# Kernel optimization log

Measured on AMD Instinct MI355X. Metric: run time of the kernel, lower is better.

The kernel has to match this reference:

```python
import jax, jax.numpy as jnp
import numpy as np

BOUND = 1.0
DENSITY_SCALE = 1.0
MIN_NEAR = 0.2
EPS = 1e-15


def setup_inputs() -> dict:
    key = jax.random.key(0)
    ks = jax.random.split(key, 10)
    N, H = 32768, 32
    rays_o = (jax.random.uniform(ks[0], (N, 3), jnp.float32) - 0.5)  # inside AABB
    rays_d = jax.random.normal(ks[1], (N, 3), jnp.float32)
    W1 = jax.random.normal(ks[2], (3, H), jnp.float32) * 0.5
    b1 = jnp.zeros((H,), jnp.float32)
    Wsig = jax.random.normal(ks[3], (H, 1), jnp.float32) * 0.5
    Wsig_d = jax.random.normal(ks[4], (H, 1), jnp.float32) * 0.5
    Wc1 = jax.random.normal(ks[5], (6, H), jnp.float32) * 0.5
    bc1 = jnp.zeros((H,), jnp.float32)
    Wc2 = jax.random.normal(ks[6], (H, 3), jnp.float32) * 0.5
    Wc2_d = jax.random.normal(ks[7], (H, 3), jnp.float32) * 0.5
    return {"rays_o": rays_o, "rays_d": rays_d, "W1": W1, "b1": b1,
            "Wsig": Wsig, "Wsig_d": Wsig_d, "Wc1": Wc1, "bc1": bc1,
            "Wc2": Wc2, "Wc2_d": Wc2_d, "num_steps": 128}


def _composite(deltas, sigma, z01, rgbs):
    # alphas / transmittance / weights, as in run()
    alphas = 1.0 - jnp.exp(-deltas * DENSITY_SCALE * sigma)           # [N,T]
    shifted = jnp.concatenate([jnp.ones_like(alphas[..., :1]),
                               1.0 - alphas + EPS], axis=-1)
    weights = alphas * jnp.cumprod(shifted, axis=-1)[..., :-1]        # [N,T]
    ws = weights.sum(axis=-1)                                          # [N]
    depth = jnp.sum(weights * z01, axis=-1)                            # [N]
    image = jnp.sum(weights[..., None] * rgbs, axis=-2)                # [N,3]
    image = image + (1.0 - ws)[..., None] * 1.0  # bg_color = 1
    return image, depth, ws


def reference(rays_o, rays_d, W1, b1, Wsig, Wsig_d, Wc1, bc1, Wc2, Wc2_d, num_steps):
    N = rays_o.shape[0]
    T = num_steps
    d = rays_d / jnp.linalg.norm(rays_d, axis=-1, keepdims=True)
    # near_far_from_aabb (slab test), aabb = [-1,1]^3
    inv = 1.0 / d
    t1 = (-BOUND - rays_o) * inv
    t2 = (BOUND - rays_o) * inv
    near = jnp.max(jnp.minimum(t1, t2), axis=-1, keepdims=True)        # [N,1]
    far = jnp.min(jnp.maximum(t1, t2), axis=-1, keepdims=True)
    near = jnp.maximum(near, MIN_NEAR)
    far = jnp.maximum(far, near + 1e-6)
    z = jnp.linspace(0.0, 1.0, T, dtype=rays_o.dtype)[None, :]
    z_vals = near + (far - near) * z                                    # [N,T]
    sample_dist = (far - near) / T                                      # [N,1]
    xyzs = rays_o[:, None, :] + d[:, None, :] * z_vals[..., None]       # [N,T,3]
    xyzs = jnp.clip(xyzs, -BOUND, BOUND)
    # surrogate density MLP (shared trunk, main + dummy heads)
    h = jax.nn.relu(jnp.einsum('ntc,ch->nth', xyzs, W1) + b1)           # [N,T,H]
    sigma = jax.nn.softplus(jnp.einsum('nth,ho->nt', h, Wsig))          # [N,T]
    sigma_dummy = jax.nn.softplus(jnp.einsum('nth,ho->nt', h, Wsig_d))
    # deltas
    deltas = z_vals[..., 1:] - z_vals[..., :-1]
    deltas = jnp.concatenate([deltas, sample_dist * jnp.ones_like(deltas[..., :1])], axis=-1)
    # surrogate color MLP on (xyz, dir)
    dirs = jnp.broadcast_to(d[:, None, :], xyzs.shape)
    feat = jnp.concatenate([xyzs, dirs], axis=-1)                       # [N,T,6]
    hc = jax.nn.relu(jnp.einsum('ntc,ch->nth', feat, Wc1) + bc1)
    rgbs = jax.nn.sigmoid(jnp.einsum('nth,hc->ntc', hc, Wc2))           # [N,T,3]
    rgbs_dummy = jax.nn.sigmoid(jnp.einsum('nth,hc->ntc', hc, Wc2_d))
    z01 = jnp.clip((z_vals - near) / (far - near), 0.0, 1.0)
    image, depth, ws = _composite(deltas, sigma, z01, rgbs)
    image_d, depth_d, _ = _composite(deltas, sigma_dummy, z01, rgbs_dummy)
    # pack: image(3) | depth(1) | weights_sum(1) | image_dummy(3) | depth_dummy(1)
    return jnp.concatenate([image, depth[:, None], ws[:, None],
                            image_d, depth_d[:, None]], axis=-1)        # [N,9]
```

## Files before the change

### kernel.cpp

```cpp
#include <hip/hip_runtime.h>
#include <hip/hip_bf16.h>


typedef float  f32x4  __attribute__((ext_vector_type(4)));
typedef short  bf16x8 __attribute__((ext_vector_type(8)));
typedef unsigned int u32;

__device__ __forceinline__ float fast_rcp(float x){ return __builtin_amdgcn_rcpf(x); }
__device__ __forceinline__ float softplus_f(float x){
    float e = __expf(-fabsf(x));
    return fmaxf(x,0.f) + __logf(1.f+e);
}
__device__ __forceinline__ float sigmoid_f(float x){ return fast_rcp(1.f+__expf(-x)); }

__device__ __forceinline__ u32 pkrn(float lo, float hi){
    const u32 a = __float_as_uint(lo) + 0x8000u;
    const u32 b = __float_as_uint(hi) + 0x8000u;
    return __builtin_amdgcn_perm(b, a, 0x07060302u);
}
__device__ __forceinline__ u32 bfr_hi(float f){
    u32 u = __float_as_uint(f);
    return (u + 0x7FFFu + ((u>>16)&1u)) & 0xFFFF0000u;
}
__device__ __forceinline__ u32 pkbf(float lo, float hi){
    return (bfr_hi(lo)>>16) | bfr_hi(hi);
}

__global__ __launch_bounds__(256)
void nerf_prep_kernel(const float* __restrict__ W1, const float* __restrict__ b1,
                      const float* __restrict__ Wsig, const float* __restrict__ Wsig_d,
                      const float* __restrict__ Wc1, const float* __restrict__ bc1,
                      const float* __restrict__ Wc2, const float* __restrict__ Wc2_d,
                      u32* __restrict__ ws)
{
    const int q0 = threadIdx.x;
#pragma unroll
    for (int k = 0; k < 6; ++k) {
        const int q = q0 + k*256;
        u32 val = 0u;
        if (q < 1024) {
            const int ut = q>>8, rem = q&255, lane = rem>>2, dw = rem&3;
            const int g = lane>>4, m = lane&15;
            if (g == 0) {
                float w[8];
                if (ut < 2) { const int u = ut*16 + m;
                    w[0]=W1[u];  w[1]=W1[32+u];  w[2]=W1[64+u];  w[3]=b1[u];
                    w[4]=0.f;    w[5]=0.f;       w[6]=0.f;       w[7]=0.f;
                } else {        const int u = (ut-2)*16 + m;
                    w[0]=Wc1[u]; w[1]=Wc1[32+u]; w[2]=Wc1[64+u]; w[3]=bc1[u];
                    w[4]=Wc1[96+u]; w[5]=Wc1[128+u]; w[6]=Wc1[160+u]; w[7]=0.f;
                }
                val = pkbf(w[2*dw], w[2*dw+1]);
            }
        } else {
            const int q2 = q-1024, ch = q2>>8, rem = q2&255, lane = rem>>2, dw = rem&3;
            const int g = lane>>4, o = lane&15;
            float w[2];
#pragma unroll
            for (int e = 0; e < 2; ++e) {
                const int kk = 2*dw + e;
                const int h = kk>>2, rr = kk&3;
                const int u_local = h*16 + g*4 + rr;
                float v = 0.f;
                if (ch == 0) {
                    if (o == 0) v = Wsig[u_local];
                    else if (o == 1) v = Wsig_d[u_local];
                } else {
                    if (o >= 2 && o <= 4) v = Wc2[u_local*3 + (o-2)];
                    else if (o >= 5 && o <= 7) v = Wc2_d[u_local*3 + (o-5)];
                }
                w[e] = v;
            }
            val = pkbf(w[0], w[1]);
        }
        ws[q] = val;
    }
}

#define PSTR 8
#define SSTR 20
#define WSTR 1792
#define CSTR 100

__global__ __launch_bounds__(512, 4)
void nerf_render_kernel(const float* __restrict__ rays_o,
                        const float* __restrict__ rays_d,
                        const u32*  __restrict__ wsm,
                        const int*  __restrict__ num_steps,
                        float* __restrict__ out,
                        int N)
{
    __shared__ u32 smem[8 * WSTR];

    const int tid  = threadIdx.x;
    const int seg  = tid>>6, lane = tid&63;
    const int ray  = blockIdx.x*64 + lane;
    const int rayc = (ray < N) ? ray : (N-1);
    const int T = num_steps[0];
    const int g = lane>>4, c = lane&15;

    u32*   posW   = smem + seg*WSTR;
    float* stashW = (float*)(smem + seg*WSTR + 64*PSTR);
    float* comb   = (float*)smem;

    const uint4* wsv = (const uint4*)wsm;
    uint4 a1u0 = wsv[0*64 + lane];
    uint4 a1u1 = wsv[1*64 + lane];
    uint4 a1u2 = wsv[2*64 + lane];
    uint4 a1u3 = wsv[3*64 + lane];
    uint4 a2u0 = wsv[256 + 0*64 + lane];
    uint4 a2u1 = wsv[256 + 1*64 + lane];
    asm volatile("" : "+v"(a1u0.x), "+v"(a1u0.y), "+v"(a1u0.z), "+v"(a1u0.w),
                      "+v"(a1u1.x), "+v"(a1u1.y), "+v"(a1u1.z), "+v"(a1u1.w),
                      "+v"(a1u2.x), "+v"(a1u2.y), "+v"(a1u2.z), "+v"(a1u2.w));
    asm volatile("" : "+v"(a1u3.x), "+v"(a1u3.y), "+v"(a1u3.z), "+v"(a1u3.w),
                      "+v"(a2u0.x), "+v"(a2u0.y), "+v"(a2u0.z), "+v"(a2u0.w),
                      "+v"(a2u1.x), "+v"(a2u1.y), "+v"(a2u1.z), "+v"(a2u1.w));

    const float ox = rays_o[rayc*3+0], oy = rays_o[rayc*3+1], oz = rays_o[rayc*3+2];
    const float rdx = rays_d[rayc*3+0], rdy = rays_d[rayc*3+1], rdz = rays_d[rayc*3+2];
    const float rn = rsqrtf(rdx*rdx + rdy*rdy + rdz*rdz);
    const float dx = rdx*rn, dy = rdy*rn, dz = rdz*rn;

    const float ix = 1.0f/dx, iy = 1.0f/dy, iz = 1.0f/dz;
    const float t1x = (-1.f-ox)*ix, t2x = (1.f-ox)*ix;
    const float t1y = (-1.f-oy)*iy, t2y = (1.f-oy)*iy;
    const float t1z = (-1.f-oz)*iz, t2z = (1.f-oz)*iz;
    float nearv = fmaxf(fmaxf(fminf(t1x,t2x), fminf(t1y,t2y)), fminf(t1z,t2z));
    float farv  = fminf(fminf(fmaxf(t1x,t2x), fmaxf(t1y,t2y)), fmaxf(t1z,t2z));
    nearv = fmaxf(nearv, 0.2f);
    farv  = fmaxf(farv, nearv + 1e-6f);

    const float span    = farv - nearv;
    const float stepz   = (T > 1) ? span/(float)(T-1) : 0.f;
    const float inv_tm1 = (T > 1) ? 1.f/(float)(T-1) : 0.f;
    const float last_dt = span/(float)T;

    const u32 dirw0 = pkbf(dx, dy);
    const u32 dirw1 = pkbf(dz, 0.f);

    const int Sper = (T + 7) >> 3;
    const int segStart = seg * Sper;
    const int segEnd = (segStart + Sper < T) ? (segStart + Sper) : T;
    const int nch = (segEnd > segStart) ? ((segEnd - segStart + 1) >> 1) : 0;

    const int posOff = 4*c;
    const int stOff  = (c>>1)*SSTR + (c&1)*8 + g*4;

    float iA0=0.f,iA1=0.f,iA2=0.f,dAc=0.f,wsA=0.f,TAx=1.f;
    float iD0=0.f,iD1=0.f,iD2=0.f,dDc=0.f,wsD=0.f,TDx=1.f;

    for (int cs = 0; cs < nch; ++cs) {
        const int t0 = segStart + cs*2;

#pragma unroll
        for (int i = 0; i < 2; ++i) {
            const float zv = fmaf(stepz, (float)(t0 + i), nearv);
            const float X = fminf(fmaxf(fmaf(dx, zv, ox), -1.f), 1.f);
            const float Y = fminf(fmaxf(fmaf(dy, zv, oy), -1.f), 1.f);
            const float Z = fminf(fmaxf(fmaf(dz, zv, oz), -1.f), 1.f);
            uint4 v;
            v.x = pkrn(X, Y);
            v.y = pkrn(Z, 1.0f);
            v.z = dirw0;
            v.w = dirw1;
            *(uint4*)&posW[lane*PSTR + i*4] = v;
        }

#define TILEB(TAU)                                                                \
        {                                                                         \
            const uint4 b1u = *(const uint4*)&posW[(TAU)*(8*PSTR) + posOff];      \
            const bf16x8 b1f = __builtin_bit_cast(bf16x8, b1u);                   \
            f32x4 acc10 = __builtin_amdgcn_mfma_f32_16x16x32_bf16(                \
                __builtin_bit_cast(bf16x8, a1u0), b1f,(f32x4){0.f,0.f,0.f,0.f},0,0,0);\
            f32x4 acc11 = __builtin_amdgcn_mfma_f32_16x16x32_bf16(                \
                __builtin_bit_cast(bf16x8, a1u1), b1f,(f32x4){0.f,0.f,0.f,0.f},0,0,0);\
            f32x4 acc12 = __builtin_amdgcn_mfma_f32_16x16x32_bf16(                \
                __builtin_bit_cast(bf16x8, a1u2), b1f,(f32x4){0.f,0.f,0.f,0.f},0,0,0);\
            f32x4 acc13 = __builtin_amdgcn_mfma_f32_16x16x32_bf16(                \
                __builtin_bit_cast(bf16x8, a1u3), b1f,(f32x4){0.f,0.f,0.f,0.f},0,0,0);\
            const u32 p00 = pkrn(fmaxf(acc10.x,0.f), fmaxf(acc10.y,0.f));         \
            const u32 p10 = pkrn(fmaxf(acc10.z,0.f), fmaxf(acc10.w,0.f));         \
            const u32 p01 = pkrn(fmaxf(acc11.x,0.f), fmaxf(acc11.y,0.f));         \
            const u32 p11 = pkrn(fmaxf(acc11.z,0.f), fmaxf(acc11.w,0.f));         \
            const u32 p02 = pkrn(fmaxf(acc12.x,0.f), fmaxf(acc12.y,0.f));         \
            const u32 p12 = pkrn(fmaxf(acc12.z,0.f), fmaxf(acc12.w,0.f));         \
            const u32 p03 = pkrn(fmaxf(acc13.x,0.f), fmaxf(acc13.y,0.f));         \
            const u32 p13 = pkrn(fmaxf(acc13.z,0.f), fmaxf(acc13.w,0.f));         \
            uint4 b2a; b2a.x = p00; b2a.y = p10; b2a.z = p01; b2a.w = p11;        \
            uint4 b2b; b2b.x = p02; b2b.y = p12; b2b.z = p03; b2b.w = p13;        \
            f32x4 acc2 = __builtin_amdgcn_mfma_f32_16x16x32_bf16(                 \
                __builtin_bit_cast(bf16x8, a2u0), __builtin_bit_cast(bf16x8, b2a),\
                (f32x4){0.f,0.f,0.f,0.f}, 0, 0, 0);                               \
            acc2 = __builtin_amdgcn_mfma_f32_16x16x32_bf16(                       \
                __builtin_bit_cast(bf16x8, a2u1), __builtin_bit_cast(bf16x8, b2b),\
                acc2, 0, 0, 0);                                                   \
            if (g < 2) {                                                          \
                *(f32x4*)&stashW[(TAU)*(8*SSTR) + stOff] = acc2;                  \
            }                                                                     \
        }
        TILEB(0) TILEB(1) TILEB(2) TILEB(3)
        TILEB(4) TILEB(5) TILEB(6) TILEB(7)
#undef TILEB

#pragma unroll
        for (int t = 0; t < 2; ++t) {
            const int tg = t0 + t;
            if (tg < segEnd) {
                const f32x4 oA = *(const f32x4*)&stashW[lane*SSTR + t*8];
                const f32x4 oB = *(const f32x4*)&stashW[lane*SSTR + t*8 + 4];
                const float dneg = (tg < T-1) ? -stepz : -last_dt;
                const float z01  = (float)tg * inv_tm1;

                const float sigA = softplus_f(oA.x);
                const float qA = __expf(dneg*sigA);
                const float wA = TAx - TAx*qA; TAx *= qA;
                iA0 = fmaf(wA, sigmoid_f(oA.z), iA0);
                iA1 = fmaf(wA, sigmoid_f(oA.w), iA1);
                iA2 = fmaf(wA, sigmoid_f(oB.x), iA2);
                dAc = fmaf(wA, z01, dAc); wsA += wA;

                const float sigD = softplus_f(oA.y);
                const float qD = __expf(dneg*sigD);
                const float wD = TDx - TDx*qD; TDx *= qD;
                iD0 = fmaf(wD, sigmoid_f(oB.y), iD0);
                iD1 = fmaf(wD, sigmoid_f(oB.z), iD1);
                iD2 = fmaf(wD, sigmoid_f(oB.w), iD2);
                dDc = fmaf(wD, z01, dDc); wsD += wD;
            }
        }
    }

    __syncthreads();
    *(f32x4*)&comb[lane*CSTR + seg*12 + 0] = (f32x4){iA0, iA1, iA2, dAc};
    *(f32x4*)&comb[lane*CSTR + seg*12 + 4] = (f32x4){wsA, TAx, iD0, iD1};
    *(f32x4*)&comb[lane*CSTR + seg*12 + 8] = (f32x4){iD2, dDc, wsD, TDx};
    __syncthreads();

    if (seg == 0) {
        float tA = TAx, tD = TDx;
#pragma unroll
        for (int s = 1; s < 8; ++s) {
            const f32x4 v0 = *(const f32x4*)&comb[lane*CSTR + s*12 + 0];
            const f32x4 v1 = *(const f32x4*)&comb[lane*CSTR + s*12 + 4];
            const f32x4 v2 = *(const f32x4*)&comb[lane*CSTR + s*12 + 8];
            iA0 = fmaf(tA, v0.x, iA0);
            iA1 = fmaf(tA, v0.y, iA1);
            iA2 = fmaf(tA, v0.z, iA2);
            dAc = fmaf(tA, v0.w, dAc);
            wsA = fmaf(tA, v1.x, wsA);
            tA *= v1.y;
            iD0 = fmaf(tD, v1.z, iD0);
            iD1 = fmaf(tD, v1.w, iD1);
            iD2 = fmaf(tD, v2.x, iD2);
            dDc = fmaf(tD, v2.y, dDc);
            wsD = fmaf(tD, v2.z, wsD);
            tD *= v2.w;
        }
        if (ray < N) {
            const float bgA = 1.f - wsA;
            const float bgD = 1.f - wsD;
            float* o = out + (size_t)ray * 9;
            o[0] = iA0 + bgA;
            o[1] = iA1 + bgA;
            o[2] = iA2 + bgA;
            o[3] = dAc;
            o[4] = wsA;
            o[5] = iD0 + bgD;
            o[6] = iD1 + bgD;
            o[7] = iD2 + bgD;
            o[8] = dDc;
        }
    }
}

extern "C" void kernel_launch(void* const* d_in, const int* in_sizes, int n_in,
                              void* d_out, int out_size, void* d_ws, size_t ws_size,
                              hipStream_t stream) {
    const float* rays_o = (const float*)d_in[0];
    const float* rays_d = (const float*)d_in[1];
    const float* W1     = (const float*)d_in[2];
    const float* b1     = (const float*)d_in[3];
    const float* Wsig   = (const float*)d_in[4];
    const float* Wsig_d = (const float*)d_in[5];
    const float* Wc1    = (const float*)d_in[6];
    const float* bc1    = (const float*)d_in[7];
    const float* Wc2    = (const float*)d_in[8];
    const float* Wc2_d  = (const float*)d_in[9];
    const int* num_steps = (const int*)d_in[10];

    const int N = in_sizes[0] / 3;
    float* out = (float*)d_out;
    u32*   ws  = (u32*)d_ws;

    hipLaunchKernelGGL(nerf_prep_kernel, dim3(1), dim3(256), 0, stream,
                       W1, b1, Wsig, Wsig_d, Wc1, bc1, Wc2, Wc2_d, ws);

    const int blocks = (N + 63) / 64;
    hipLaunchKernelGGL(nerf_render_kernel, dim3(blocks), dim3(512), 0, stream,
                       rays_o, rays_d, ws, num_steps, out, N);
}
```

Measured before the change: 57.24 us.

## Split ray samples across two blocks and combine partials in separate kernel

The render kernel now uses 256-thread blocks, each handling half of the sample range of 64 rays. Partial composite state (accumulations plus transmittance) goes to workspace, and a new combine kernel merges the two halves. The aim is smaller blocks, higher occupancy and more blocks for scheduling. The cost is an extra kernel launch and a round trip of the partials through global memory. The ReLU/pack code is also rewritten using vector max, which is cosmetic.

```diff
diff --git a/kernel.cpp b/kernel.cpp
--- a/kernel.cpp
+++ b/kernel.cpp
@@ -80,21 +80,23 @@
 #define PSTR 8
 #define SSTR 20
 #define WSTR 1792
-#define CSTR 100
-
-__global__ __launch_bounds__(512, 4)
+#define CSTR 52
+#define PART_OFF 2048
+
+__global__ __launch_bounds__(256, 5)
 void nerf_render_kernel(const float* __restrict__ rays_o,
                         const float* __restrict__ rays_d,
                         const u32*  __restrict__ wsm,
                         const int*  __restrict__ num_steps,
-                        float* __restrict__ out,
+                        float* __restrict__ partials,
                         int N)
 {
-    __shared__ u32 smem[8 * WSTR];
+    __shared__ u32 smem[4 * WSTR];
 
     const int tid  = threadIdx.x;
     const int seg  = tid>>6, lane = tid&63;
-    const int ray  = blockIdx.x*64 + lane;
+    const int half = blockIdx.x & 1;
+    const int ray  = (blockIdx.x >> 1)*64 + lane;
     const int rayc = (ray < N) ? ray : (N-1);
     const int T = num_steps[0];
     const int g = lane>>4, c = lane&15;
@@ -139,9 +141,12 @@
     const u32 dirw0 = pkbf(dx, dy);
     const u32 dirw1 = pkbf(dz, 0.f);
 
-    const int Sper = (T + 7) >> 3;
-    const int segStart = seg * Sper;
-    const int segEnd = (segStart + Sper < T) ? (segStart + Sper) : T;
+    const int halfT = (T + 1) >> 1;
+    const int Sper  = (halfT + 3) >> 2;
+    const int hEnd  = ((half + 1)*halfT < T) ? (half + 1)*halfT : T;
+    const int segStart = half*halfT + seg*Sper;
+    int segEnd = segStart + Sper;
+    segEnd = (segEnd < hEnd) ? segEnd : hEnd;
     const int nch = (segEnd > segStart) ? ((segEnd - segStart + 1) >> 1) : 0;
 
     const int posOff = 4*c;
@@ -149,6 +154,7 @@
 
     float iA0=0.f,iA1=0.f,iA2=0.f,dAc=0.f,wsA=0.f,TAx=1.f;
     float iD0=0.f,iD1=0.f,iD2=0.f,dDc=0.f,wsD=0.f,TDx=1.f;
+    const f32x4 z4 = {0.f,0.f,0.f,0.f};
 
     for (int cs = 0; cs < nch; ++cs) {
         const int t0 = segStart + cs*2;
@@ -172,26 +178,25 @@
             const uint4 b1u = *(const uint4*)&posW[(TAU)*(8*PSTR) + posOff];      \
             const bf16x8 b1f = __builtin_bit_cast(bf16x8, b1u);                   \
             f32x4 acc10 = __builtin_amdgcn_mfma_f32_16x16x32_bf16(                \
-                __builtin_bit_cast(bf16x8, a1u0), b1f,(f32x4){0.f,0.f,0.f,0.f},0,0,0);\
+                __builtin_bit_cast(bf16x8, a1u0), b1f, z4, 0,0,0);                \
             f32x4 acc11 = __builtin_amdgcn_mfma_f32_16x16x32_bf16(                \
-                __builtin_bit_cast(bf16x8, a1u1), b1f,(f32x4){0.f,0.f,0.f,0.f},0,0,0);\
+                __builtin_bit_cast(bf16x8, a1u1), b1f, z4, 0,0,0);                \
             f32x4 acc12 = __builtin_amdgcn_mfma_f32_16x16x32_bf16(                \
-                __builtin_bit_cast(bf16x8, a1u2), b1f,(f32x4){0.f,0.f,0.f,0.f},0,0,0);\
+                __builtin_bit_cast(bf16x8, a1u2), b1f, z4, 0,0,0);                \
             f32x4 acc13 = __builtin_amdgcn_mfma_f32_16x16x32_bf16(                \
-                __builtin_bit_cast(bf16x8, a1u3), b1f,(f32x4){0.f,0.f,0.f,0.f},0,0,0);\
-            const u32 p00 = pkrn(fmaxf(acc10.x,0.f), fmaxf(acc10.y,0.f));         \
-            const u32 p10 = pkrn(fmaxf(acc10.z,0.f), fmaxf(acc10.w,0.f));         \
-            const u32 p01 = pkrn(fmaxf(acc11.x,0.f), fmaxf(acc11.y,0.f));         \
-            const u32 p11 = pkrn(fmaxf(acc11.z,0.f), fmaxf(acc11.w,0.f));         \
-            const u32 p02 = pkrn(fmaxf(acc12.x,0.f), fmaxf(acc12.y,0.f));         \
-            const u32 p12 = pkrn(fmaxf(acc12.z,0.f), fmaxf(acc12.w,0.f));         \
-            const u32 p03 = pkrn(fmaxf(acc13.x,0.f), fmaxf(acc13.y,0.f));         \
-            const u32 p13 = pkrn(fmaxf(acc13.z,0.f), fmaxf(acc13.w,0.f));         \
-            uint4 b2a; b2a.x = p00; b2a.y = p10; b2a.z = p01; b2a.w = p11;        \
-            uint4 b2b; b2b.x = p02; b2b.y = p12; b2b.z = p03; b2b.w = p13;        \
+                __builtin_bit_cast(bf16x8, a1u3), b1f, z4, 0,0,0);                \
+            const f32x4 r0 = __builtin_elementwise_max(acc10, z4);                \
+            const f32x4 r1 = __builtin_elementwise_max(acc11, z4);                \
+            const f32x4 r2 = __builtin_elementwise_max(acc12, z4);                \
+            const f32x4 r3 = __builtin_elementwise_max(acc13, z4);                \
+            uint4 b2a, b2b;                                                       \
+            b2a.x = pkrn(r0.x, r0.y);  b2a.y = pkrn(r0.z, r0.w);                  \
+            b2a.z = pkrn(r1.x, r1.y);  b2a.w = pkrn(r1.z, r1.w);                  \
+            b2b.x = pkrn(r2.x, r2.y);  b2b.y = pkrn(r2.z, r2.w);                  \
+            b2b.z = pkrn(r3.x, r3.y);  b2b.w = pkrn(r3.z, r3.w);                  \
             f32x4 acc2 = __builtin_amdgcn_mfma_f32_16x16x32_bf16(                 \
                 __builtin_bit_cast(bf16x8, a2u0), __builtin_bit_cast(bf16x8, b2a),\
-                (f32x4){0.f,0.f,0.f,0.f}, 0, 0, 0);                               \
+                z4, 0, 0, 0);                                                     \
             acc2 = __builtin_amdgcn_mfma_f32_16x16x32_bf16(                       \
                 __builtin_bit_cast(bf16x8, a2u1), __builtin_bit_cast(bf16x8, b2b),\
                 acc2, 0, 0, 0);                                                   \
@@ -237,10 +242,10 @@
     *(f32x4*)&comb[lane*CSTR + seg*12 + 8] = (f32x4){iD2, dDc, wsD, TDx};
     __syncthreads();
 
-    if (seg == 0) {
+    if (seg == 0 && ray < N) {
         float tA = TAx, tD = TDx;
 #pragma unroll
-        for (int s = 1; s < 8; ++s) {
+        for (int s = 1; s < 4; ++s) {
             const f32x4 v0 = *(const f32x4*)&comb[lane*CSTR + s*12 + 0];
             const f32x4 v1 = *(const f32x4*)&comb[lane*CSTR + s*12 + 4];
             const f32x4 v2 = *(const f32x4*)&comb[lane*CSTR + s*12 + 8];
@@ -257,21 +262,52 @@
             wsD = fmaf(tD, v2.z, wsD);
             tD *= v2.w;
         }
-        if (ray < N) {
-            const float bgA = 1.f - wsA;
-            const float bgD = 1.f - wsD;
-            float* o = out + (size_t)ray * 9;
-            o[0] = iA0 + bgA;
-            o[1] = iA1 + bgA;
-            o[2] = iA2 + bgA;
-            o[3] = dAc;
-            o[4] = wsA;
-            o[5] = iD0 + bgD;
-            o[6] = iD1 + bgD;
-            o[7] = iD2 + bgD;
-            o[8] = dDc;
-        }
+        float* pw = partials + (size_t)(half*N + ray)*12;
+        *(f32x4*)&pw[0] = (f32x4){iA0, iA1, iA2, dAc};
+        *(f32x4*)&pw[4] = (f32x4){wsA, tA, iD0, iD1};
+        *(f32x4*)&pw[8] = (f32x4){iD2, dDc, wsD, tD};
     }
+}
+
+__global__ __launch_bounds__(256)
+void nerf_combine_kernel(const float* __restrict__ partials,
+                         float* __restrict__ out, int N)
+{
+    const int ray = blockIdx.x*256 + threadIdx.x;
+    if (ray >= N) return;
+    const float* p0 = partials + (size_t)ray*12;
+    const float* p1 = partials + (size_t)(N + ray)*12;
+    const f32x4 a0 = *(const f32x4*)&p0[0];
+    const f32x4 a1 = *(const f32x4*)&p0[4];
+    const f32x4 a2 = *(const f32x4*)&p0[8];
+    const f32x4 b0 = *(const f32x4*)&p1[0];
+    const f32x4 b1 = *(const f32x4*)&p1[4];
+    const f32x4 b2 = *(const f32x4*)&p1[8];
+
+    const float TA0 = a1.y, TD0 = a2.w;
+    const float iA0 = a0.x + TA0*b0.x;
+    const float iA1 = a0.y + TA0*b0.y;
+    const float iA2 = a0.z + TA0*b0.z;
+    const float dAc = a0.w + TA0*b0.w;
+    const float wsA = a1.x + TA0*b1.x;
+    const float iD0 = a1.z + TD0*b1.z;
+    const float iD1 = a1.w + TD0*b1.w;
+    const float iD2 = a2.x + TD0*b2.x;
+    const float dDc = a2.y + TD0*b2.y;
+    const float wsD = a2.z + TD0*b2.z;
+
+    const float bgA = 1.f - wsA;
+    const float bgD = 1.f - wsD;
+    float* o = out + (size_t)ray * 9;
+    o[0] = iA0 + bgA;
+    o[1] = iA1 + bgA;
+    o[2] = iA2 + bgA;
+    o[3] = dAc;
+    o[4] = wsA;
+    o[5] = iD0 + bgD;
+    o[6] = iD1 + bgD;
+    o[7] = iD2 + bgD;
+    o[8] = dDc;
 }
 
 extern "C" void kernel_launch(void* const* d_in, const int* in_sizes, int n_in,
@@ -292,11 +328,16 @@
     const int N = in_sizes[0] / 3;
     float* out = (float*)d_out;
     u32*   ws  = (u32*)d_ws;
+    float* partials = (float*)((u32*)d_ws + PART_OFF);
 
     hipLaunchKernelGGL(nerf_prep_kernel, dim3(1), dim3(256), 0, stream,
                        W1, b1, Wsig, Wsig_d, Wc1, bc1, Wc2, Wc2_d, ws);
 
-    const int blocks = (N + 63) / 64;
-    hipLaunchKernelGGL(nerf_render_kernel, dim3(blocks), dim3(512), 0, stream,
-                       rays_o, rays_d, ws, num_steps, out, N);
-}
+    const int rblocks = ((N + 63) / 64) * 2;
+    hipLaunchKernelGGL(nerf_render_kernel, dim3(rblocks), dim3(256), 0, stream,
+                       rays_o, rays_d, ws, num_steps, partials, N);
+
+    const int cblocks = (N + 255) / 256;
+    hipLaunchKernelGGL(nerf_combine_kernel, dim3(cblocks), dim3(256), 0, stream,
+                       partials, out, N);
+}
```

Result: slower. 59.86 us (+4.6%).
